# Performance work log

Measured on AMD Instinct MI355X. Metric: run time of the kernel, lower is better.

The kernel has to match this reference:

```python
import jax, jax.numpy as jnp
import numpy as np

B, T, D, H = 4, 2048, 1024, 16
HD = D // H  # head_dim = 64


def setup_inputs() -> dict:
    key = jax.random.key(0)
    ks = jax.random.split(key, 5)
    s = 0.02
    return {
        "x": jax.random.normal(ks[0], (B, T, D), dtype=jnp.float32),
        "Wq": jax.random.normal(ks[1], (D, D), dtype=jnp.float32) * s,
        "Wk": jax.random.normal(ks[2], (D, D), dtype=jnp.float32) * s,
        "Wv": jax.random.normal(ks[3], (D, D), dtype=jnp.float32) * s,
        "Wp": jax.random.normal(ks[4], (D, D), dtype=jnp.float32) * s,
    }


def reference(x, Wq, Wk, Wv, Wp):
    b, t, d = x.shape
    # QKV projections (bias=False), reshape to (b, h, t, hd)
    q = (x @ Wq.T).reshape(b, t, H, HD).transpose(0, 2, 1, 3)
    k = (x @ Wk.T).reshape(b, t, H, HD).transpose(0, 2, 1, 3)
    v = (x @ Wv.T).reshape(b, t, H, HD).transpose(0, 2, 1, 3)
    # scaled scores with causal mask
    scores = jnp.einsum("bhqd,bhkd->bhqk", q, k) / jnp.sqrt(jnp.float32(HD))
    causal = jnp.triu(jnp.ones((t, t), dtype=bool), k=1)
    scores = jnp.where(causal, -jnp.inf, scores)
    weights = jax.nn.softmax(scores, axis=-1)
    # dropout = 0.0 / eval mode -> identity
    ctx = jnp.einsum("bhqk,bhkd->bhqd", weights, v)
    ctx = ctx.transpose(0, 2, 1, 3).reshape(b, t, d)
    return ctx @ Wp.T
```

## Files before the change

kernel.cpp:

```cpp
#include <hip/hip_runtime.h>

typedef unsigned short u16;
typedef unsigned int u32;
typedef __attribute__((ext_vector_type(8))) short short8;
typedef __attribute__((ext_vector_type(4))) short short4_t;
typedef __attribute__((ext_vector_type(4))) float float4_t;

#define T_SEQ 2048
#define DMODEL 1024
#define NH 16
#define HD 64

#define GLL16(g, l) __builtin_amdgcn_global_load_lds( \
    (const __attribute__((address_space(1))) u32*)(g), \
    (__attribute__((address_space(3))) u32*)(l), 16, 0, 0)

#define PH_BAR() do { asm volatile("" ::: "memory"); \
    __builtin_amdgcn_s_barrier(); \
    asm volatile("" ::: "memory"); } while (0)
#define WAIT_LGKM0() asm volatile("s_waitcnt lgkmcnt(0)" ::: "memory")
#define WAIT_VM4() asm volatile("s_waitcnt vmcnt(4)" ::: "memory")
#define WAIT_VM0() asm volatile("s_waitcnt vmcnt(0)" ::: "memory")

__device__ inline u16 f2b(float f) {
  u32 x = __builtin_bit_cast(u32, f);
  x += 0x7fffu + ((x >> 16) & 1u);
  return (u16)(x >> 16);
}

__global__ __launch_bounds__(256) void conv_f2b(
    const float* __restrict__ x, const float* __restrict__ wq,
    const float* __restrict__ wk, const float* __restrict__ wv,
    const float* __restrict__ wp, u16* __restrict__ xb, u16* __restrict__ wb) {
  const size_t SZc = (size_t)8192 * 1024, WSZc = (size_t)1024 * 1024;
  size_t i = ((size_t)blockIdx.x * 256 + threadIdx.x) * 8;
  const float* s; u16* d; size_t off;
  if (i < SZc) { s = x; d = xb; off = i; }
  else {
    size_t j = i - SZc;
    size_t w = j >> 20;
    off = j & (WSZc - 1);
    s = (w == 0) ? wq : (w == 1) ? wk : (w == 2) ? wv : wp;
    d = wb + w * WSZc;
  }
  float4_t a = *(const float4_t*)(s + off);
  float4_t b = *(const float4_t*)(s + off + 4);
  short8 o;
  o[0] = (short)f2b(a[0]); o[1] = (short)f2b(a[1]);
  o[2] = (short)f2b(a[2]); o[3] = (short)f2b(a[3]);
  o[4] = (short)f2b(b[0]); o[5] = (short)f2b(b[1]);
  o[6] = (short)f2b(b[2]); o[7] = (short)f2b(b[3]);
  *(short8*)(d + off) = o;
}

__global__ __launch_bounds__(256) void gemm_bt(
    const u16* __restrict__ A,
    const u16* __restrict__ B0, const u16* __restrict__ B1, const u16* __restrict__ B2,
    u16* __restrict__ C0, u16* __restrict__ C1, u16* __restrict__ C2,
    float* __restrict__ Cf,
    int N, int Kd, int vtz, int of32, int scz, float cscale)
{
  const u16* Bp = (blockIdx.z == 0) ? B0 : ((blockIdx.z == 1) ? B1 : B2);
  u16* Cp = (blockIdx.z == 0) ? C0 : ((blockIdx.z == 1) ? C1 : C2);
  const bool vt = ((int)blockIdx.z == vtz);
  const float cs = ((int)blockIdx.z == scz) ? cscale : 1.0f;
  __shared__ u16 As[128 * 32];
  __shared__ u16 Bs[128 * 32];
  const int tid = threadIdx.x;
  const int lane = tid & 63;
  const int li = lane & 15;
  const int quad = lane >> 4;
  const int wv = tid >> 6;
  const int wm = (wv >> 1) * 64;
  const int wn = (wv & 1) * 64;
  const size_t bm = (size_t)blockIdx.x * 128;
  const size_t bn = (size_t)blockIdx.y * 128;

  float4_t acc[4][4];
  const float4_t z4 = {0.f, 0.f, 0.f, 0.f};
#pragma unroll
  for (int i = 0; i < 4; i++)
#pragma unroll
    for (int j = 0; j < 4; j++) acc[i][j] = z4;

  const int c0 = tid, c1 = tid + 256;
  const int r0 = c0 >> 2, e0 = (c0 & 3) * 8;
  const int r1 = c1 >> 2, e1 = (c1 & 3) * 8;

  for (int k0 = 0; k0 < Kd; k0 += 32) {
    __syncthreads();
    GLL16(A + (bm + r0) * Kd + k0 + e0, &As[c0 * 8]);
    GLL16(A + (bm + r1) * Kd + k0 + e1, &As[c1 * 8]);
    GLL16(Bp + (bn + r0) * Kd + k0 + e0, &Bs[c0 * 8]);
    GLL16(Bp + (bn + r1) * Kd + k0 + e1, &Bs[c1 * 8]);
    __syncthreads();
    short8 af[4], bf[4];
#pragma unroll
    for (int i = 0; i < 4; i++)
      af[i] = *(const short8*)&As[(wm + i * 16 + li) * 32 + quad * 8];
#pragma unroll
    for (int j = 0; j < 4; j++)
      bf[j] = *(const short8*)&Bs[(wn + j * 16 + li) * 32 + quad * 8];
#pragma unroll
    for (int i = 0; i < 4; i++)
#pragma unroll
      for (int j = 0; j < 4; j++)
        acc[i][j] = __builtin_amdgcn_mfma_f32_16x16x32_bf16(bf[j], af[i], acc[i][j], 0, 0, 0);
  }

  if (of32) {
#pragma unroll
    for (int i = 0; i < 4; i++)
#pragma unroll
      for (int j = 0; j < 4; j++) {
        size_t row = bm + wm + (size_t)(i * 16 + li);
        size_t col = bn + wn + (size_t)(j * 16 + quad * 4);
        *(float4_t*)&Cf[row * (size_t)N + col] = acc[i][j];
      }
  } else if (!vt) {
#pragma unroll
    for (int i = 0; i < 4; i++)
#pragma unroll
      for (int j = 0; j < 4; j++) {
        size_t row = bm + wm + (size_t)(i * 16 + li);
        size_t col = bn + wn + (size_t)(j * 16 + quad * 4);
        short4_t o;
#pragma unroll
        for (int r = 0; r < 4; r++) o[r] = (short)f2b(acc[i][j][r] * cs);
        *(short4_t*)&Cp[row * (size_t)N + col] = o;
      }
  } else {
#pragma unroll
    for (int i = 0; i < 4; i++) {
      size_t row = bm + wm + (size_t)(i * 16 + li);
      size_t bb = row >> 11;
      size_t tt = row & 2047;
#pragma unroll
      for (int j = 0; j < 4; j++) {
        size_t col = bn + wn + (size_t)(j * 16 + quad * 4);
#pragma unroll
        for (int r = 0; r < 4; r++)
          Cp[(bb * 1024 + col + r) * 2048 + tt] = f2b(acc[i][j][r]);
      }
    }
  }
}

__global__ __launch_bounds__(512, 2) void gemm_qkv(
    const u16* __restrict__ Ap,
    const u16* __restrict__ B0w, const u16* __restrict__ B1w,
    const u16* __restrict__ B2w,
    u16* __restrict__ C0, u16* __restrict__ C1, u16* __restrict__ C2,
    float sc) {
  __shared__ u16 Als[2][2][8192];
  __shared__ u16 Bls[2][2][8192];
  const int z = blockIdx.z;
  const u16* __restrict__ Bp = (z == 0) ? B0w : (z == 1) ? B1w : B2w;
  u16* __restrict__ Cp = (z == 0) ? C0 : (z == 1) ? C1 : C2;
  const float cs = (z == 0) ? sc : 1.0f;
  const int tid = threadIdx.x;
  const int lane = tid & 63;
  const int li = lane & 15;
  const int quad = lane >> 4;
  const int wid = tid >> 6;
  const int wr = wid >> 2;
  const int wc = wid & 3;
  const size_t bm = (size_t)blockIdx.x * 256;
  const size_t bn = (size_t)blockIdx.y * 256;

  const int xs0 = (quad ^ (li & 7)) * 16;
  const int lrA = wr * 64 + li;
  const int lrB = wc * 32 + li;

  const int srow = tid >> 3;
  const int cswz8 = ((tid & 7) ^ (srow & 7)) * 8;

  auto stageA = [&](int db, int h, int tk) {
#pragma unroll
    for (int u = 0; u < 2; ++u) {
      int lr = u * 64 + srow;
      size_t grow = bm + (size_t)((lr >> 6) * 128 + h * 64 + (lr & 63));
      GLL16(Ap + grow * 1024 + (size_t)(tk * 64) + cswz8,
            &Als[db][h][u * 4096 + tid * 8]);
    }
  };
  auto stageB = [&](int db, int p, int tk) {
#pragma unroll
    for (int u = 0; u < 2; ++u) {
      int lr = u * 64 + srow;
      size_t grow = bn + (size_t)((lr >> 5) * 64 + p * 32 + (lr & 31));
      GLL16(Bp + grow * 1024 + (size_t)(tk * 64) + cswz8,
            &Bls[db][p][u * 4096 + tid * 8]);
    }
  };

  float4_t acc[8][4];
  const float4_t z4 = {0.f, 0.f, 0.f, 0.f};
#pragma unroll
  for (int i = 0; i < 8; ++i)
#pragma unroll
    for (int j = 0; j < 4; ++j) acc[i][j] = z4;

  short8 af[2][4], bf0[2][2], bf1[2][2];

#define LDA(DB, H) \
  { const char* base = (const char*)&Als[DB][H][0]; \
    _Pragma("unroll") for (int ii = 0; ii < 4; ++ii) { \
      af[0][ii] = *(const short8*)(base + (size_t)(lrA + ii * 16) * 128 + xs0); \
      af[1][ii] = *(const short8*)(base + (size_t)(lrA + ii * 16) * 128 + (xs0 ^ 64)); } }
#define LDB(DB, P, BF) \
  { const char* base = (const char*)&Bls[DB][P][0]; \
    _Pragma("unroll") for (int jj = 0; jj < 2; ++jj) { \
      BF[0][jj] = *(const short8*)(base + (size_t)(lrB + jj * 16) * 128 + xs0); \
      BF[1][jj] = *(const short8*)(base + (size_t)(lrB + jj * 16) * 128 + (xs0 ^ 64)); } }
#define MFMA16(I0, J0, BF) \
  __builtin_amdgcn_s_setprio(1); \
  _Pragma("unroll") for (int ii = 0; ii < 4; ++ii) \
  _Pragma("unroll") for (int jj = 0; jj < 2; ++jj) \
  _Pragma("unroll") for (int ks = 0; ks < 2; ++ks) \
    acc[I0 + ii][J0 + jj] = __builtin_amdgcn_mfma_f32_16x16x32_bf16( \
        BF[ks][jj], af[ks][ii], acc[I0 + ii][J0 + jj], 0, 0, 0); \
  __builtin_amdgcn_s_setprio(0)

  stageA(0, 0, 0); stageB(0, 0, 0); stageA(0, 1, 0); stageB(0, 1, 0);
  stageA(1, 0, 1); stageB(1, 1, 1);
  WAIT_VM4();
  PH_BAR();

  const int NT = 16;
#pragma unroll 1
  for (int it = 0; it < 8; ++it) {
    const int t1 = 2 * it + 1, t2 = 2 * it + 2, t3 = 2 * it + 3;
    const bool s2 = (t2 < NT), s3 = (t3 < NT);

    LDA(0, 0); LDB(0, 0, bf0);
    stageA(1, 1, t1);
    PH_BAR(); WAIT_LGKM0();
    MFMA16(0, 0, bf0);
    PH_BAR();
    LDB(0, 1, bf1);
    stageB(1, 0, t1);
    PH_BAR(); WAIT_LGKM0();
    MFMA16(0, 2, bf1);
    PH_BAR();
    LDA(0, 1);
    if (s2) stageA(0, 0, t2);
    PH_BAR(); WAIT_LGKM0();
    MFMA16(4, 2, bf1);
    PH_BAR();
    if (s2) { stageB(0, 1, t2); WAIT_VM4(); } else { WAIT_VM0(); }
    PH_BAR();
    MFMA16(4, 0, bf0);
    PH_BAR();

    LDA(1, 0); LDB(1, 0, bf0);
    if (s2) stageA(0, 1, t2);
    PH_BAR(); WAIT_LGKM0();
    MFMA16(0, 0, bf0);
    PH_BAR();
    LDB(1, 1, bf1);
    if (s2) stageB(0, 0, t2);
    PH_BAR(); WAIT_LGKM0();
    MFMA16(0, 2, bf1);
    PH_BAR();
    LDA(1, 1);
    if (s3) stageA(1, 0, t3);
    PH_BAR(); WAIT_LGKM0();
    MFMA16(4, 2, bf1);
    PH_BAR();
    if (s3) { stageB(1, 1, t3); WAIT_VM4(); } else { WAIT_VM0(); }
    PH_BAR();
    MFMA16(4, 0, bf0);
    PH_BAR();
  }
#undef LDA
#undef LDB
#undef MFMA16

  const size_t colb = bn + (size_t)wc * 64;
  if (z != 2) {
#pragma unroll
    for (int i = 0; i < 8; ++i) {
      const size_t row = bm + (size_t)(wr * 128 + i * 16 + li);
#pragma unroll
      for (int j = 0; j < 4; ++j) {
        const size_t col = colb + (size_t)(j * 16 + quad * 4);
        short4_t o;
#pragma unroll
        for (int r = 0; r < 4; ++r) o[r] = (short)f2b(acc[i][j][r] * cs);
        *(short4_t*)&Cp[row * 1024 + col] = o;
      }
    }
  } else {
#pragma unroll
    for (int i = 0; i < 8; ++i) {
      const size_t row = bm + (size_t)(wr * 128 + i * 16 + li);
      const size_t bb = row >> 11;
      const size_t tt = row & 2047;
#pragma unroll
      for (int j = 0; j < 4; ++j) {
        const size_t col = colb + (size_t)(j * 16 + quad * 4);
#pragma unroll
        for (int r = 0; r < 4; ++r)
          Cp[(bb * 1024 + col + r) * 2048 + tt] = f2b(acc[i][j][r]);
      }
    }
  }
}

#define LROW 72
__global__ __launch_bounds__(512) void attn_fwd(const u16* __restrict__ Qb,
                                                const u16* __restrict__ Kb,
                                                const u16* __restrict__ Vtb,
                                                u16* __restrict__ Ob) {
  __shared__ u16 Qs[128 * LROW];
  __shared__ u16 Kds[2][64 * LROW];
  __shared__ u16 Vds[2][64 * LROW];
  const int bh = blockIdx.y;
  const int bidx = bh >> 4;
  const int tid = threadIdx.x;
  const int lane = tid & 63;
  const int wv = tid >> 6;
  const int li = lane & 15;
  const int quad = lane >> 4;
  const size_t qkBase = ((size_t)bidx * T_SEQ) * DMODEL + (size_t)(bh & 15) * HD;
  const size_t vBase = (size_t)bh * HD * T_SEQ;
  const int krow = tid >> 3;
  const int kc8 = (tid & 7) * 8;
  const int kld = krow * LROW + kc8;
  const float4_t z4 = {0.f, 0.f, 0.f, 0.f};

#pragma unroll 1
  for (int ph = 0; ph < 2; ph++) {
    const int qblk = ph ? (int)blockIdx.x : (15 - (int)blockIdx.x);
    const int q0 = qblk * 128;
    const int ktmax = 2 * qblk + 1;
    const int qg0 = q0 + wv * 16;

    __syncthreads();
#pragma unroll
    for (int t = 0; t < 4; t++) {
      int slot = tid + t * 512;
      int row = slot >> 4, hc = slot & 15;
      *(short4_t*)&Qs[row * LROW + hc * 4] =
          *(const short4_t*)&Qb[qkBase + (size_t)(q0 + row) * DMODEL + hc * 4];
    }
    short8 kpre = *(const short8*)&Kb[qkBase + (size_t)krow * DMODEL + kc8];
    short8 vpre = *(const short8*)&Vtb[vBase + (size_t)krow * T_SEQ + kc8];
    __syncthreads();
    short8 qf[2];
    {
      const int row = wv * 16 + li;
#pragma unroll
      for (int s = 0; s < 2; s++)
        qf[s] = *(const short8*)&Qs[row * LROW + s * 32 + quad * 8];
    }
    *(short8*)&Kds[0][kld] = kpre;
    *(short8*)&Vds[0][kld] = vpre;
    kpre = *(const short8*)&Kb[qkBase + (size_t)(64 + krow) * DMODEL + kc8];
    vpre = *(const short8*)&Vtb[vBase + (size_t)krow * T_SEQ + 64 + kc8];

    float4_t accO[4];
#pragma unroll
    for (int dt = 0; dt < 4; dt++) accO[dt] = z4;
    float l_i = 0.f;

    for (int kt = 0; kt <= ktmax; kt++) {
      const int k0 = kt * 64;
      const int cb = kt & 1;
      __syncthreads();
      if (kt < ktmax) {
        *(short8*)&Kds[cb ^ 1][kld] = kpre;
        *(short8*)&Vds[cb ^ 1][kld] = vpre;
        if (kt + 1 < ktmax) {
          const int kn = k0 + 128;
          kpre = *(const short8*)&Kb[qkBase + (size_t)(kn + krow) * DMODEL + kc8];
          vpre = *(const short8*)&Vtb[vBase + (size_t)krow * T_SEQ + kn + kc8];
        }
      }
      if (k0 > qg0 + 15) continue;

      float4_t st[4];
#pragma unroll
      for (int jt = 0; jt < 4; jt++) {
        float4_t c4 = z4;
        const int row = jt * 16 + li;
#pragma unroll
        for (int s = 0; s < 2; s++) {
          short8 kf = *(const short8*)&Kds[cb][row * LROW + s * 32 + quad * 8];
          c4 = __builtin_amdgcn_mfma_f32_16x16x32_bf16(kf, qf[s], c4, 0, 0, 0);
        }
        st[jt] = c4;
      }

      short4_t pf[4];
      if (k0 + 63 > qg0) {
        const int ig = qg0 + li;
#pragma unroll
        for (int jt = 0; jt < 4; jt++)
#pragma unroll
          for (int r = 0; r < 4; r++) {
            int jg = k0 + jt * 16 + quad * 4 + r;
            float p = (jg <= ig) ? __builtin_amdgcn_exp2f(st[jt][r]) : 0.f;
            l_i += p;
            pf[jt][r] = (short)(__builtin_bit_cast(u32, p) >> 16);
          }
      } else {
#pragma unroll
        for (int jt = 0; jt < 4; jt++)
#pragma unroll
          for (int r = 0; r < 4; r++) {
            float p = __builtin_amdgcn_exp2f(st[jt][r]);
            l_i += p;
            pf[jt][r] = (short)(__builtin_bit_cast(u32, p) >> 16);
          }
      }

#pragma unroll
      for (int dt = 0; dt < 4; dt++) {
        const int d = dt * 16 + li;
#pragma unroll
        for (int jt = 0; jt < 4; jt++) {
          short4_t vf = *(const short4_t*)&Vds[cb][d * LROW + jt * 16 + quad * 4];
          accO[dt] = __builtin_amdgcn_mfma_f32_16x16x16bf16_1k(vf, pf[jt], accO[dt], 0, 0, 0);
        }
      }
    }

    l_i += __shfl_xor(l_i, 16);
    l_i += __shfl_xor(l_i, 32);
    const float inv = 1.f / l_i;
    const int orow = q0 + wv * 16 + li;
    const size_t obase = ((size_t)bidx * T_SEQ + orow) * DMODEL + (size_t)(bh & 15) * HD;
#pragma unroll
    for (int dt = 0; dt < 4; dt++) {
      short4_t o4;
#pragma unroll
      for (int r = 0; r < 4; r++) o4[r] = (short)f2b(accO[dt][r] * inv);
      *(short4_t*)&Ob[obase + dt * 16 + quad * 4] = o4;
    }
  }
}

extern "C" void kernel_launch(void* const* d_in, const int* in_sizes, int n_in,
                              void* d_out, int out_size, void* d_ws, size_t ws_size,
                              hipStream_t stream) {
  (void)in_sizes; (void)n_in; (void)out_size; (void)ws_size;
  const float* x  = (const float*)d_in[0];
  const float* Wq = (const float*)d_in[1];
  const float* Wk = (const float*)d_in[2];
  const float* Wv = (const float*)d_in[3];
  const float* Wp = (const float*)d_in[4];
  float* out = (float*)d_out;

  const size_t SZ  = (size_t)8192 * 1024;
  const size_t WSZ = (size_t)1024 * 1024;

  u16* xb  = (u16*)d_ws;
  u16* wb  = xb + SZ;
  u16* Q   = wb + 4 * WSZ;
  u16* Kp  = Q + SZ;
  u16* Vt  = Kp + SZ;
  u16* ctx = Vt + SZ;

  const float SC = 0.18033688011112042f;

  dim3 blk(256);
  conv_f2b<<<dim3((unsigned)((SZ + 4 * WSZ) / 8 / 256)), blk, 0, stream>>>(
      x, Wq, Wk, Wv, Wp, xb, wb);
  gemm_qkv<<<dim3(32, 4, 3), dim3(512), 0, stream>>>(
      xb, wb, wb + WSZ, wb + 2 * WSZ, Q, Kp, Vt, SC);
  attn_fwd<<<dim3(8, 4 * NH), dim3(512), 0, stream>>>(Q, Kp, Vt, ctx);
  gemm_bt<<<dim3(64, 8, 1), blk, 0, stream>>>(
      ctx, wb + 3 * WSZ, nullptr, nullptr, nullptr, nullptr, nullptr, out,
      DMODEL, DMODEL, -1, 1, -1, 1.0f);
}
```

Baseline: 251.1 us.

## Load Q fragments directly, pack P with cvt_pk_bf16, raise attention occupancy

```diff
diff --git a/kernel.cpp b/kernel.cpp
--- a/kernel.cpp
+++ b/kernel.cpp
@@ -5,6 +5,7 @@
 typedef __attribute__((ext_vector_type(8))) short short8;
 typedef __attribute__((ext_vector_type(4))) short short4_t;
 typedef __attribute__((ext_vector_type(4))) float float4_t;
+typedef __attribute__((ext_vector_type(2))) unsigned int uint2_t;
 
 #define T_SEQ 2048
 #define DMODEL 1024
@@ -309,11 +310,10 @@
 }
 
 #define LROW 72
-__global__ __launch_bounds__(512) void attn_fwd(const u16* __restrict__ Qb,
-                                                const u16* __restrict__ Kb,
-                                                const u16* __restrict__ Vtb,
-                                                u16* __restrict__ Ob) {
-  __shared__ u16 Qs[128 * LROW];
+__global__ __launch_bounds__(512, 4) void attn_fwd(const u16* __restrict__ Qb,
+                                                   const u16* __restrict__ Kb,
+                                                   const u16* __restrict__ Vtb,
+                                                   u16* __restrict__ Ob) {
   __shared__ u16 Kds[2][64 * LROW];
   __shared__ u16 Vds[2][64 * LROW];
   const int bh = blockIdx.y;
@@ -338,23 +338,15 @@
     const int qg0 = q0 + wv * 16;
 
     __syncthreads();
-#pragma unroll
-    for (int t = 0; t < 4; t++) {
-      int slot = tid + t * 512;
-      int row = slot >> 4, hc = slot & 15;
-      *(short4_t*)&Qs[row * LROW + hc * 4] =
-          *(const short4_t*)&Qb[qkBase + (size_t)(q0 + row) * DMODEL + hc * 4];
+
+    short8 qf[2];
+    {
+      const u16* qrow = Qb + qkBase + (size_t)(q0 + wv * 16 + li) * DMODEL;
+      qf[0] = *(const short8*)(qrow + quad * 8);
+      qf[1] = *(const short8*)(qrow + 32 + quad * 8);
     }
     short8 kpre = *(const short8*)&Kb[qkBase + (size_t)krow * DMODEL + kc8];
     short8 vpre = *(const short8*)&Vtb[vBase + (size_t)krow * T_SEQ + kc8];
-    __syncthreads();
-    short8 qf[2];
-    {
-      const int row = wv * 16 + li;
-#pragma unroll
-      for (int s = 0; s < 2; s++)
-        qf[s] = *(const short8*)&Qs[row * LROW + s * 32 + quad * 8];
-    }
     *(short8*)&Kds[0][kld] = kpre;
     *(short8*)&Vds[0][kld] = vpre;
     kpre = *(const short8*)&Kb[qkBase + (size_t)(64 + krow) * DMODEL + kc8];
@@ -363,7 +355,7 @@
     float4_t accO[4];
 #pragma unroll
     for (int dt = 0; dt < 4; dt++) accO[dt] = z4;
-    float l_i = 0.f;
+    float l0 = 0.f, l1 = 0.f;
 
     for (int kt = 0; kt <= ktmax; kt++) {
       const int k0 = kt * 64;
@@ -397,23 +389,35 @@
       if (k0 + 63 > qg0) {
         const int ig = qg0 + li;
 #pragma unroll
-        for (int jt = 0; jt < 4; jt++)
+        for (int jt = 0; jt < 4; jt++) {
+          float p[4];
 #pragma unroll
           for (int r = 0; r < 4; r++) {
             int jg = k0 + jt * 16 + quad * 4 + r;
-            float p = (jg <= ig) ? __builtin_amdgcn_exp2f(st[jt][r]) : 0.f;
-            l_i += p;
-            pf[jt][r] = (short)(__builtin_bit_cast(u32, p) >> 16);
+            p[r] = (jg <= ig) ? __builtin_amdgcn_exp2f(st[jt][r]) : 0.f;
           }
+          l0 += p[0] + p[1];
+          l1 += p[2] + p[3];
+          u32 lo, hi;
+          asm("v_cvt_pk_bf16_f32 %0, %1, %2" : "=v"(lo) : "v"(p[0]), "v"(p[1]));
+          asm("v_cvt_pk_bf16_f32 %0, %1, %2" : "=v"(hi) : "v"(p[2]), "v"(p[3]));
+          uint2_t w = {lo, hi};
+          pf[jt] = __builtin_bit_cast(short4_t, w);
+        }
       } else {
 #pragma unroll
-        for (int jt = 0; jt < 4; jt++)
-#pragma unroll
-          for (int r = 0; r < 4; r++) {
-            float p = __builtin_amdgcn_exp2f(st[jt][r]);
-            l_i += p;
-            pf[jt][r] = (short)(__builtin_bit_cast(u32, p) >> 16);
-          }
+        for (int jt = 0; jt < 4; jt++) {
+          float p[4];
+#pragma unroll
+          for (int r = 0; r < 4; r++) p[r] = __builtin_amdgcn_exp2f(st[jt][r]);
+          l0 += p[0] + p[1];
+          l1 += p[2] + p[3];
+          u32 lo, hi;
+          asm("v_cvt_pk_bf16_f32 %0, %1, %2" : "=v"(lo) : "v"(p[0]), "v"(p[1]));
+          asm("v_cvt_pk_bf16_f32 %0, %1, %2" : "=v"(hi) : "v"(p[2]), "v"(p[3]));
+          uint2_t w = {lo, hi};
+          pf[jt] = __builtin_bit_cast(short4_t, w);
+        }
       }
 
 #pragma unroll
@@ -427,6 +431,7 @@
       }
     }
 
+    float l_i = l0 + l1;
     l_i += __shfl_xor(l_i, 16);
     l_i += __shfl_xor(l_i, 32);
     const float inv = 1.f / l_i;
```

Measured after the change: 250.9 us. No clear change (-0.1%).
